# Performance work log

Hardware: AMD Instinct MI355X
Metric: run time of the kernel (lower is better)

The kernel has to match this reference:

```python
import jax, jax.numpy as jnp
import numpy as np

NX, NY = 8192, 8192
FX, FY = 1024, 1024
EMB, EMB_OUT = 512, 512


def setup_inputs() -> dict:
    key = jax.random.key(0)
    ks = jax.random.split(key, 8)
    s = lambda f: 1.0 / np.sqrt(f)
    return {
        "x": jax.random.normal(ks[0], (NX, FX), jnp.float32),
        "y": jax.random.normal(ks[1], (NY, FY), jnp.float32),
        "Wx": jax.random.uniform(ks[2], (FX, EMB), jnp.float32, -s(FX), s(FX)),
        "bx": jax.random.uniform(ks[3], (EMB,), jnp.float32, -s(FX), s(FX)),
        "Wy": jax.random.uniform(ks[4], (FY, EMB), jnp.float32, -s(FY), s(FY)),
        "by": jax.random.uniform(ks[5], (EMB,), jnp.float32, -s(FY), s(FY)),
        "Wg": jax.random.uniform(ks[6], (EMB, EMB_OUT), jnp.float32, -s(EMB), s(EMB)),
        "bg": jax.random.uniform(ks[7], (EMB_OUT,), jnp.float32, -s(EMB), s(EMB)),
    }


def reference(x, y, Wx, bx, Wy, by, Wg, bg):
    # Linear projections: [Nx, emb], [Ny, emb]
    xp = x @ Wx + bx
    yp = y @ Wy + by
    # Pairwise affinity (Dice-coefficient style normalization)
    A_ = xp @ yp.T                              # [Nx, Ny]
    Dcol = jnp.sum(xp * xp, axis=1)[:, None]    # ||x_i||^2, diag of xp@xp.T
    Drow = jnp.sum(yp * yp, axis=1)[None, :]    # ||y_j||^2, diag of yp@yp.T
    A = 2.0 * A_ / (Dcol + Drow)                # [Nx, Ny]
    # Weighted aggregation over x nodes, then ReLU MLP
    gwf = A.T @ xp                              # [Ny, emb]
    return jax.nn.relu(gwf @ Wg + bg)           # [Ny, emb_out]
```

## Files before the change

kernel.cpp:

```cpp
#include <hip/hip_runtime.h>
#include <hip/hip_bf16.h>


typedef __attribute__((ext_vector_type(8))) short bf16x8;
typedef __attribute__((ext_vector_type(4))) short bf16x4;
typedef __attribute__((ext_vector_type(4))) float f32x4;

__device__ __forceinline__ short f2b(float f) {
    unsigned int u = __builtin_bit_cast(unsigned int, f);
    unsigned int r = (u + 0x7fffu + ((u >> 16) & 1u)) >> 16;
    return (short)r;
}
__device__ __forceinline__ float b2f(short s) {
    unsigned int u = ((unsigned int)(unsigned short)s) << 16;
    return __builtin_bit_cast(float, u);
}

__device__ __forceinline__ void cp16(const void* g, void* l) {
    __builtin_amdgcn_global_load_lds(
        (const __attribute__((address_space(1))) void*)g,
        (__attribute__((address_space(3))) void*)l, 16, 0, 0);
}

template<int N>
__device__ __forceinline__ void waitvm() {
    if constexpr (N == 0)       asm volatile("s_waitcnt vmcnt(0)" ::: "memory");
    else if constexpr (N == 2)  asm volatile("s_waitcnt vmcnt(2)" ::: "memory");
    else if constexpr (N == 3)  asm volatile("s_waitcnt vmcnt(3)" ::: "memory");
    else if constexpr (N == 4)  asm volatile("s_waitcnt vmcnt(4)" ::: "memory");
    else if constexpr (N == 6)  asm volatile("s_waitcnt vmcnt(6)" ::: "memory");
    else if constexpr (N == 8)  asm volatile("s_waitcnt vmcnt(8)" ::: "memory");
    else if constexpr (N == 12) asm volatile("s_waitcnt vmcnt(12)" ::: "memory");
    else static_assert(N == 0, "unsupported vmcnt literal");
}

__device__ __forceinline__ int gslot(int c, int row) {
    return c ^ (row & 3) ^ ((row >> 2) & 3);
}

constexpr int EPI_XP = 0;
constexpr int EPI_BF = 1;
constexpr int EPI_AT = 2;

template<int EPI, int TM, int TN, int RING>
__device__ __forceinline__ void gemm_deep(
    const short* __restrict__ A, int lda,
    const short* __restrict__ Bt, int ldb,
    int N, int K, int bm, int bn, int kbase,
    const float* __restrict__ bias,
    short* __restrict__ outb,
    float* __restrict__ Dacc,
    const float* __restrict__ Drow, const float* __restrict__ Dcol)
{
    constexpr int FRM = TM / 32;
    constexpr int FRN = TN / 32;
    constexpr int CPA = TM * 4 / 256;
    constexpr int CPB = TN * 4 / 256;
    constexpr int CPT = CPA + CPB;
    __shared__ __align__(16) short As[RING][TM * 32];
    __shared__ __align__(16) short Bs[RING][TN * 32];

    const int tid  = threadIdx.x;
    const int wave = tid >> 6;
    const int lane = tid & 63;
    const int quad = lane >> 4;
    const int l15  = lane & 15;
    const int wm   = (wave >> 1) * (FRM * 16);
    const int wn   = (wave & 1) * (FRN * 16);
    const int nk   = K / 32;

    f32x4 acc[FRM][FRN];
#pragma unroll
    for (int i = 0; i < FRM; i++)
#pragma unroll
        for (int j = 0; j < FRN; j++) acc[i][j] = f32x4{0.f, 0.f, 0.f, 0.f};

    auto stage = [&](int slot, int t) {
        const int k0 = kbase + t * 32;
#pragma unroll
        for (int s = 0; s < CPA; s++) {
            const int seg = tid + 256 * s;
            const int row = seg >> 2, c8 = seg & 3;
            const int gg  = gslot(c8, row);
            cp16(&A[(size_t)(bm + row) * lda + k0 + gg * 8], &As[slot][seg * 8]);
        }
#pragma unroll
        for (int s = 0; s < CPB; s++) {
            const int seg = tid + 256 * s;
            const int row = seg >> 2, c8 = seg & 3;
            const int gg  = gslot(c8, row);
            cp16(&Bt[(size_t)(bn + row) * ldb + k0 + gg * 8], &Bs[slot][seg * 8]);
        }
    };

    bf16x8 a[FRM], b[FRN];
    auto ldfrag = [&](int slot) {
#pragma unroll
        for (int i = 0; i < FRM; i++) {
            const int row = wm + i * 16 + l15;
            a[i] = *(const bf16x8*)&As[slot][row * 32 + (gslot(quad, row) << 3)];
        }
#pragma unroll
        for (int j = 0; j < FRN; j++) {
            const int row = wn + j * 16 + l15;
            b[j] = *(const bf16x8*)&Bs[slot][row * 32 + (gslot(quad, row) << 3)];
        }
    };

#pragma unroll
    for (int p = 0; p < RING - 1; ++p) stage(p, p);
    if constexpr (RING == 3) waitvm<CPT>(); else waitvm<2 * CPT>();
    __builtin_amdgcn_s_barrier();
    __builtin_amdgcn_sched_barrier(0);
    ldfrag(0);

    for (int t = 0; t < nk; ++t) {
        __builtin_amdgcn_s_setprio(1);
#pragma unroll
        for (int i = 0; i < FRM; i++)
#pragma unroll
            for (int j = 0; j < FRN; j++)
                acc[i][j] = __builtin_amdgcn_mfma_f32_16x16x32_bf16(a[i], b[j], acc[i][j], 0, 0, 0);
        __builtin_amdgcn_s_setprio(0);

        if (t + 1 < nk) {
            if constexpr (RING == 3) {
                waitvm<0>();
            } else {
                if (t + 2 < nk) waitvm<CPT>(); else waitvm<0>();
            }
            __builtin_amdgcn_s_barrier();
            __builtin_amdgcn_sched_barrier(0);
            ldfrag((t + 1) % RING);
            if (t + RING - 1 < nk)
                stage((t + RING - 1) % RING, t + RING - 1);
        }
    }

#pragma unroll
    for (int im = 0; im < FRM; ++im) {
#pragma unroll
        for (int r = 0; r < 4; ++r) {
            const int gm = bm + wm + im * 16 + quad * 4 + r;
            if (EPI == EPI_XP) {
                float s = 0.f;
#pragma unroll
                for (int jn = 0; jn < FRN; ++jn) {
                    const int gn = bn + wn + jn * 16 + l15;
                    const float v = acc[im][jn][r] + bias[gn];
                    outb[(size_t)gm * N + gn] = f2b(v);
                    s += v * v;
                }
#pragma unroll
                for (int m = 1; m < 16; m <<= 1) s += __shfl_xor(s, m, 64);
                if (l15 == 0) atomicAdd(&Dacc[gm], s);
            } else if (EPI == EPI_AT) {
                const float dy = Drow[gm];
#pragma unroll
                for (int jn = 0; jn < FRN; ++jn) {
                    const int gn = bn + wn + jn * 16 + l15;
                    const float v = 2.f * acc[im][jn][r] * __builtin_amdgcn_rcpf(Dcol[gn] + dy);
                    outb[(size_t)gm * N + gn] = f2b(v);
                }
            } else {
#pragma unroll
                for (int jn = 0; jn < FRN; ++jn) {
                    const int gn = bn + wn + jn * 16 + l15;
                    outb[(size_t)gm * N + gn] = f2b(acc[im][jn][r]);
                }
            }
        }
    }
}

__global__ __launch_bounds__(256, 3)
void k_proj(const short* __restrict__ A, const short* __restrict__ Bt,
            const float* __restrict__ bias, short* __restrict__ outb,
            float* __restrict__ Dacc)
{
    gemm_deep<EPI_XP, 64, 128, 4>(A, 1024, Bt, 1024, 512, 1024,
                                  blockIdx.y * 64, blockIdx.x * 128, 0,
                                  bias, outb, Dacc, nullptr, nullptr);
}

__global__ __launch_bounds__(256, 4)
void k_zT(const short* __restrict__ WgT, const short* __restrict__ xpb,
          short* __restrict__ zT)
{
    gemm_deep<EPI_BF, 64, 128, 3>(WgT, 512, xpb, 512, 8192, 512,
                                  blockIdx.y * 64, blockIdx.x * 128, 0,
                                  nullptr, zT, nullptr, nullptr, nullptr);
}

__global__ __launch_bounds__(256, 3)
void k_aff(const short* __restrict__ ypb, const short* __restrict__ xpb,
           short* __restrict__ At, const float* __restrict__ Dy,
           const float* __restrict__ Dx)
{
    const int flat = blockIdx.x;
    const int xcd = flat & 7;
    const int q   = flat >> 3;
    const int by  = xcd * 8 + (q & 7);
    const int bx  = q >> 3;
    gemm_deep<EPI_AT, 128, 128, 3>(ypb, 512, xpb, 512, 8192, 512,
                                   by * 128, bx * 128, 0,
                                   nullptr, At, nullptr, Dy, Dx);
}

__global__ __launch_bounds__(256, 2)
void k_agg(const short* __restrict__ At, const short* __restrict__ zT,
           short* __restrict__ p0, short* __restrict__ p1)
{
    const int flat = blockIdx.x;
    const int xcd = flat & 7;
    const int q   = flat >> 3;
    const int g   = xcd * 16 + (q >> 2);
    const int bm  = (g >> 1) * 128;
    const int z   = g & 1;
    const int bn  = (q & 3) * 128;
    short* outb = z ? p1 : p0;
    gemm_deep<EPI_BF, 128, 128, 4>(At, 8192, zT, 8192, 512, 4096,
                                   bm, bn, z * 4096,
                                   nullptr, outb, nullptr, nullptr, nullptr);
}

__global__ __launch_bounds__(256)
void k_fin(const short* __restrict__ p0, const short* __restrict__ p1,
           const float* __restrict__ bg, float* __restrict__ out)
{
    const int idx = (blockIdx.x * 256 + threadIdx.x) * 8;
    const int col = idx & 511;
    const bf16x8 a = *(const bf16x8*)&p0[idx];
    const bf16x8 b = *(const bf16x8*)&p1[idx];
    const f32x4 g0 = *(const f32x4*)&bg[col];
    const f32x4 g1 = *(const f32x4*)&bg[col + 4];
    f32x4 o0, o1;
#pragma unroll
    for (int e = 0; e < 4; ++e) {
        o0[e] = fmaxf(b2f(a[e]) + b2f(b[e]) + g0[e], 0.f);
        o1[e] = fmaxf(b2f(a[e + 4]) + b2f(b[e + 4]) + g1[e], 0.f);
    }
    *(f32x4*)&out[idx]     = o0;
    *(f32x4*)&out[idx + 4] = o1;
}

__global__ __launch_bounds__(256)
void k_cvt(const float* __restrict__ x, const float* __restrict__ y,
           short* __restrict__ xb, short* __restrict__ yb)
{
    const float* in  = blockIdx.y ? y  : x;
    short*       out = blockIdx.y ? yb : xb;
    const int i = (blockIdx.x * 256 + threadIdx.x) * 4;
    const float4 v = *(const float4*)&in[i];
    bf16x4 b;
    b[0] = f2b(v.x); b[1] = f2b(v.y); b[2] = f2b(v.z); b[3] = f2b(v.w);
    *(bf16x4*)&out[i] = b;
}

__device__ __forceinline__ void transpose_body(
    const float* __restrict__ in, short* __restrict__ out, int R, int C)
{
    __shared__ short t[32][33];
    const int tx = threadIdx.x, ty = threadIdx.y;
    const int bx = blockIdx.x * 32, by = blockIdx.y * 32;
#pragma unroll
    for (int i = 0; i < 32; i += 8)
        t[ty + i][tx] = f2b(in[(size_t)(by + ty + i) * C + bx + tx]);
    __syncthreads();
#pragma unroll
    for (int i = 0; i < 32; i += 8)
        out[(size_t)(bx + ty + i) * R + by + tx] = t[tx][ty + i];
}

__global__ __launch_bounds__(256)
void t_wxy(const float* __restrict__ Wx, const float* __restrict__ Wy,
           short* __restrict__ WxT, short* __restrict__ WyT)
{
    transpose_body(blockIdx.z ? Wy : Wx, blockIdx.z ? WyT : WxT, 1024, 512);
}

__global__ __launch_bounds__(256)
void t_wg(const float* __restrict__ Wg, short* __restrict__ WgT)
{
    transpose_body(Wg, WgT, 512, 512);
}

extern "C" void kernel_launch(void* const* d_in, const int* in_sizes, int n_in,
                              void* d_out, int out_size, void* d_ws, size_t ws_size,
                              hipStream_t stream)
{
    const float* x  = (const float*)d_in[0];
    const float* y  = (const float*)d_in[1];
    const float* Wx = (const float*)d_in[2];
    const float* bx = (const float*)d_in[3];
    const float* Wy = (const float*)d_in[4];
    const float* by = (const float*)d_in[5];
    const float* Wg = (const float*)d_in[6];
    const float* bg = (const float*)d_in[7];
    float* out = (float*)d_out;

    char* p = (char*)d_ws;
    short* At   = (short*)p;
    short* xb   = (short*)p;
    short* yb   = (short*)(p + (size_t)8192 * 1024 * 2);
    p += (size_t)8192 * 8192 * 2;
    short* xpb  = (short*)p; p += (size_t)8192 * 512 * 2;
    short* ypb  = (short*)p; p += (size_t)8192 * 512 * 2;
    short* zT   = (short*)p; p += (size_t)512 * 8192 * 2;
    short* WxT  = (short*)p; p += (size_t)512 * 1024 * 2;
    short* WyT  = (short*)p; p += (size_t)512 * 1024 * 2;
    short* WgT  = (short*)p; p += (size_t)512 * 512 * 2;
    float* Dx   = (float*)p; p += (size_t)8192 * 4;
    float* Dy   = (float*)p; p += (size_t)8192 * 4;
    short* p0 = xpb;
    short* p1 = ypb;

    hipMemsetAsync(Dx, 0, 2 * 8192 * sizeof(float), stream);

    dim3 tb(32, 8);
    t_wxy<<<dim3(16, 32, 2), tb, 0, stream>>>(Wx, Wy, WxT, WyT);
    t_wg<<<dim3(16, 16), tb, 0, stream>>>(Wg, WgT);

    k_cvt<<<dim3(8192, 2), 256, 0, stream>>>(x, y, xb, yb);

    k_proj<<<dim3(4, 128), 256, 0, stream>>>(xb, WxT, bx, xpb, Dx);
    k_proj<<<dim3(4, 128), 256, 0, stream>>>(yb, WyT, by, ypb, Dy);

    k_zT<<<dim3(64, 8), 256, 0, stream>>>(WgT, xpb, zT);

    k_aff<<<4096, 256, 0, stream>>>(ypb, xpb, At, Dy, Dx);

    k_agg<<<512, 256, 0, stream>>>(At, zT, p0, p1);

    k_fin<<<2048, 256, 0, stream>>>(p0, p1, bg, out);
}
```

Baseline: 362.9 us.

## Use per-wave private LDS pipeline for affinity GEMM and issue prefetch before MFMAs

```diff
diff --git a/kernel.cpp b/kernel.cpp
--- a/kernel.cpp
+++ b/kernel.cpp
@@ -33,6 +33,9 @@
     else if constexpr (N == 12) asm volatile("s_waitcnt vmcnt(12)" ::: "memory");
     else static_assert(N == 0, "unsupported vmcnt literal");
 }
+__device__ __forceinline__ void waitlgkm0() {
+    asm volatile("s_waitcnt lgkmcnt(0)" ::: "memory");
+}
 
 __device__ __forceinline__ int gslot(int c, int row) {
     return c ^ (row & 3) ^ ((row >> 2) & 3);
@@ -49,8 +52,7 @@
     int N, int K, int bm, int bn, int kbase,
     const float* __restrict__ bias,
     short* __restrict__ outb,
-    float* __restrict__ Dacc,
-    const float* __restrict__ Drow, const float* __restrict__ Dcol)
+    float* __restrict__ Dacc)
 {
     constexpr int FRM = TM / 32;
     constexpr int FRN = TN / 32;
@@ -81,15 +83,15 @@
         for (int s = 0; s < CPA; s++) {
             const int seg = tid + 256 * s;
             const int row = seg >> 2, c8 = seg & 3;
-            const int gg  = gslot(c8, row);
-            cp16(&A[(size_t)(bm + row) * lda + k0 + gg * 8], &As[slot][seg * 8]);
+            cp16(&A[(size_t)(bm + row) * lda + k0 + gslot(c8, row) * 8],
+                 &As[slot][seg * 8]);
         }
 #pragma unroll
         for (int s = 0; s < CPB; s++) {
             const int seg = tid + 256 * s;
             const int row = seg >> 2, c8 = seg & 3;
-            const int gg  = gslot(c8, row);
-            cp16(&Bt[(size_t)(bn + row) * ldb + k0 + gg * 8], &Bs[slot][seg * 8]);
+            cp16(&Bt[(size_t)(bn + row) * ldb + k0 + gslot(c8, row) * 8],
+                 &Bs[slot][seg * 8]);
         }
     };
 
@@ -109,12 +111,15 @@
 
 #pragma unroll
     for (int p = 0; p < RING - 1; ++p) stage(p, p);
-    if constexpr (RING == 3) waitvm<CPT>(); else waitvm<2 * CPT>();
+    waitvm<(RING - 2) * CPT>();
     __builtin_amdgcn_s_barrier();
     __builtin_amdgcn_sched_barrier(0);
     ldfrag(0);
 
     for (int t = 0; t < nk; ++t) {
+        if (t + RING - 1 < nk)
+            stage((t + RING - 1) % RING, t + RING - 1);
+
         __builtin_amdgcn_s_setprio(1);
 #pragma unroll
         for (int i = 0; i < FRM; i++)
@@ -125,15 +130,15 @@
 
         if (t + 1 < nk) {
             if constexpr (RING == 3) {
-                waitvm<0>();
+                if (t + 2 < nk) waitvm<CPT>(); else waitvm<0>();
             } else {
-                if (t + 2 < nk) waitvm<CPT>(); else waitvm<0>();
+                if (t + 3 < nk)      waitvm<2 * CPT>();
+                else if (t + 2 < nk) waitvm<CPT>();
+                else                 waitvm<0>();
             }
             __builtin_amdgcn_s_barrier();
             __builtin_amdgcn_sched_barrier(0);
             ldfrag((t + 1) % RING);
-            if (t + RING - 1 < nk)
-                stage((t + RING - 1) % RING, t + RING - 1);
         }
     }
 
@@ -154,14 +159,6 @@
 #pragma unroll
                 for (int m = 1; m < 16; m <<= 1) s += __shfl_xor(s, m, 64);
                 if (l15 == 0) atomicAdd(&Dacc[gm], s);
-            } else if (EPI == EPI_AT) {
-                const float dy = Drow[gm];
-#pragma unroll
-                for (int jn = 0; jn < FRN; ++jn) {
-                    const int gn = bn + wn + jn * 16 + l15;
-                    const float v = 2.f * acc[im][jn][r] * __builtin_amdgcn_rcpf(Dcol[gn] + dy);
-                    outb[(size_t)gm * N + gn] = f2b(v);
-                }
             } else {
 #pragma unroll
                 for (int jn = 0; jn < FRN; ++jn) {
@@ -173,6 +170,105 @@
     }
 }
 
+__device__ __forceinline__ void gemm_wavep_aff(
+    const short* __restrict__ A,
+    const short* __restrict__ Bt,
+    int bm, int bn,
+    short* __restrict__ At,
+    const float* __restrict__ Dy, const float* __restrict__ Dx)
+{
+    constexpr int FRM = 4, FRN = 4, NK = 16;
+    __shared__ __align__(16) short Ls[4][2][2][64 * 32];
+
+    const int tid  = threadIdx.x;
+    const int wave = tid >> 6;
+    const int lane = tid & 63;
+    const int quad = lane >> 4;
+    const int l15  = lane & 15;
+    const int wm   = (wave >> 1) * 64;
+    const int wn   = (wave & 1) * 64;
+
+    f32x4 acc[FRM][FRN];
+#pragma unroll
+    for (int i = 0; i < FRM; i++)
+#pragma unroll
+        for (int j = 0; j < FRN; j++) acc[i][j] = f32x4{0.f, 0.f, 0.f, 0.f};
+
+    auto stage = [&](int slot, int t) {
+        const int k0 = t * 32;
+#pragma unroll
+        for (int s = 0; s < 4; s++) {
+            const int seg = s * 64 + lane;
+            const int row = seg >> 2, c8 = seg & 3;
+            cp16(&A[(size_t)(bm + wm + row) * 512 + k0 + gslot(c8, row) * 8],
+                 &Ls[wave][slot][0][seg * 8]);
+        }
+#pragma unroll
+        for (int s = 0; s < 4; s++) {
+            const int seg = s * 64 + lane;
+            const int row = seg >> 2, c8 = seg & 3;
+            cp16(&Bt[(size_t)(bn + wn + row) * 512 + k0 + gslot(c8, row) * 8],
+                 &Ls[wave][slot][1][seg * 8]);
+        }
+    };
+
+    bf16x8 a[FRM], b[FRN];
+    auto ldfrag = [&](int slot) {
+#pragma unroll
+        for (int i = 0; i < FRM; i++) {
+            const int row = i * 16 + l15;
+            a[i] = *(const bf16x8*)&Ls[wave][slot][0][row * 32 + (gslot(quad, row) << 3)];
+        }
+#pragma unroll
+        for (int j = 0; j < FRN; j++) {
+            const int row = j * 16 + l15;
+            b[j] = *(const bf16x8*)&Ls[wave][slot][1][row * 32 + (gslot(quad, row) << 3)];
+        }
+    };
+
+    stage(0, 0);
+    stage(1, 1);
+    waitvm<8>();
+    __builtin_amdgcn_sched_barrier(0);
+    ldfrag(0);
+
+    for (int t = 0; t < NK; ++t) {
+        if (t + 2 < NK) {
+            waitlgkm0();
+            __builtin_amdgcn_sched_barrier(0);
+            stage(t & 1, t + 2);
+        }
+        __builtin_amdgcn_s_setprio(1);
+#pragma unroll
+        for (int i = 0; i < FRM; i++)
+#pragma unroll
+            for (int j = 0; j < FRN; j++)
+                acc[i][j] = __builtin_amdgcn_mfma_f32_16x16x32_bf16(a[i], b[j], acc[i][j], 0, 0, 0);
+        __builtin_amdgcn_s_setprio(0);
+
+        if (t + 1 < NK) {
+            if (t + 2 < NK) waitvm<8>(); else waitvm<0>();
+            __builtin_amdgcn_sched_barrier(0);
+            ldfrag((t + 1) & 1);
+        }
+    }
+
+#pragma unroll
+    for (int im = 0; im < FRM; ++im) {
+#pragma unroll
+        for (int r = 0; r < 4; ++r) {
+            const int gm = bm + wm + im * 16 + quad * 4 + r;
+            const float dy = Dy[gm];
+#pragma unroll
+            for (int jn = 0; jn < FRN; ++jn) {
+                const int gn = bn + wn + jn * 16 + l15;
+                const float v = 2.f * acc[im][jn][r] * __builtin_amdgcn_rcpf(Dx[gn] + dy);
+                At[(size_t)gm * 8192 + gn] = f2b(v);
+            }
+        }
+    }
+}
+
 __global__ __launch_bounds__(256, 3)
 void k_proj(const short* __restrict__ A, const short* __restrict__ Bt,
             const float* __restrict__ bias, short* __restrict__ outb,
@@ -180,7 +276,7 @@
 {
     gemm_deep<EPI_XP, 64, 128, 4>(A, 1024, Bt, 1024, 512, 1024,
                                   blockIdx.y * 64, blockIdx.x * 128, 0,
-                                  bias, outb, Dacc, nullptr, nullptr);
+                                  bias, outb, Dacc);
 }
 
 __global__ __launch_bounds__(256, 4)
@@ -189,10 +285,10 @@
 {
     gemm_deep<EPI_BF, 64, 128, 3>(WgT, 512, xpb, 512, 8192, 512,
                                   blockIdx.y * 64, blockIdx.x * 128, 0,
-                                  nullptr, zT, nullptr, nullptr, nullptr);
-}
-
-__global__ __launch_bounds__(256, 3)
+                                  nullptr, zT, nullptr);
+}
+
+__global__ __launch_bounds__(256, 2)
 void k_aff(const short* __restrict__ ypb, const short* __restrict__ xpb,
            short* __restrict__ At, const float* __restrict__ Dy,
            const float* __restrict__ Dx)
@@ -202,9 +298,7 @@
     const int q   = flat >> 3;
     const int by  = xcd * 8 + (q & 7);
     const int bx  = q >> 3;
-    gemm_deep<EPI_AT, 128, 128, 3>(ypb, 512, xpb, 512, 8192, 512,
-                                   by * 128, bx * 128, 0,
-                                   nullptr, At, nullptr, Dy, Dx);
+    gemm_wavep_aff(ypb, xpb, by * 128, bx * 128, At, Dy, Dx);
 }
 
 __global__ __launch_bounds__(256, 2)
@@ -221,7 +315,7 @@
     short* outb = z ? p1 : p0;
     gemm_deep<EPI_BF, 128, 128, 4>(At, 8192, zT, 8192, 512, 4096,
                                    bm, bn, z * 4096,
-                                   nullptr, outb, nullptr, nullptr, nullptr);
+                                   nullptr, outb, nullptr);
 }
 
 __global__ __launch_bounds__(256)
```

After: 366.3 us. Within noise of the previous version (+0.9%).
